# Kernel tuning notes

Measured on AMD Instinct MI355X. Metric: run time of the kernel, lower is better.

## Reference

```python
import jax, jax.numpy as jnp
import numpy as np

RMS_EPS = 1.1920928955078125e-07  # torch.finfo(float32).eps, nn.RMSNorm default when eps=None


def setup_inputs() -> dict:
    key = jax.random.key(0)
    ks = jax.random.split(key, 7)
    B, T, C, Wh, E, K = 8, 4096, 256, 1024, 8, 2
    return {
        "x": jax.random.normal(ks[0], (B, T, C), dtype=jnp.float32),
        "rms_weight": jnp.ones((C,), dtype=jnp.float32),
        "W1": jax.random.normal(ks[1], (E, C, Wh), dtype=jnp.float32),
        "b1": jax.random.normal(ks[2], (E, Wh), dtype=jnp.float32),
        "W2": jax.random.normal(ks[3], (E, Wh, C), dtype=jnp.float32),
        "b2": jax.random.normal(ks[4], (E, C), dtype=jnp.float32),
        "expert_ids": jax.random.randint(ks[5], (B, T, K), 0, E, dtype=jnp.int64),
    }


def reference(x, rms_weight, W1, b1, W2, b2, expert_ids):
    # RMSNorm over last dim (torch nn.RMSNorm, eps = float32 eps)
    xn = x * jax.lax.rsqrt(jnp.mean(x * x, axis=-1, keepdims=True) + RMS_EPS) * rms_weight
    # Per-expert 2-layer MLP. The torch code gathers per-token weight copies then bmm's;
    # mathematically identical (and far cheaper in memory) is: run every expert densely,
    # then gather the K selected expert outputs per token.
    h = jax.nn.gelu(jnp.einsum("btc,ecw->btew", xn, W1) + b1, approximate=False)  # [B,T,E,Wh]
    y = jnp.einsum("btew,ewc->btec", h, W2) + b2  # [B,T,E,C]
    # gather selected experts: [B,T,K,C]; dropout p is 0.0 (eval) -> identity
    out = jnp.take_along_axis(y, expert_ids[..., None], axis=2)
    return out
```

## Files before the change

kernel.cpp:

```cpp
#include <hip/hip_runtime.h>
#include <cstdint>

typedef unsigned short ushort_t;
typedef __bf16 bf16x8 __attribute__((ext_vector_type(8)));
typedef ushort_t u16x8 __attribute__((ext_vector_type(8)));
typedef float f32x4 __attribute__((ext_vector_type(4)));
typedef uint32_t u32x4 __attribute__((ext_vector_type(4)));

#define RMS_EPS 1.1920928955078125e-07f

__device__ __forceinline__ ushort_t f2bf(float f) {
  uint32_t u = __builtin_bit_cast(uint32_t, f);
  u += 0x7fffu + ((u >> 16) & 1u);
  return (ushort_t)(u >> 16);
}

__device__ __forceinline__ void g2l16(const ushort_t* g, ushort_t* l) {
  __builtin_amdgcn_global_load_lds(
      (const __attribute__((address_space(1))) uint32_t*)g,
      (__attribute__((address_space(3))) uint32_t*)l, 16, 0, 0);
}

__global__ void rmsnorm_cast(const float* __restrict__ x, const float* __restrict__ w,
                             ushort_t* __restrict__ xn) {
  int token = blockIdx.x * 4 + (threadIdx.x >> 6);
  int lane = threadIdx.x & 63;
  const float4* row = reinterpret_cast<const float4*>(x + (size_t)token * 256);
  float4 v = row[lane];
  float s = v.x * v.x + v.y * v.y + v.z * v.z + v.w * v.w;
#pragma unroll
  for (int off = 1; off < 64; off <<= 1) s += __shfl_xor(s, off);
  float inv = rsqrtf(s * (1.0f / 256.0f) + RMS_EPS);
  const float4* wr = reinterpret_cast<const float4*>(w);
  float4 wv = wr[lane];
  ushort4 o;
  o.x = f2bf(v.x * inv * wv.x);
  o.y = f2bf(v.y * inv * wv.y);
  o.z = f2bf(v.z * inv * wv.z);
  o.w = f2bf(v.w * inv * wv.w);
  *reinterpret_cast<ushort4*>(xn + (size_t)token * 256 + lane * 4) = o;
}

__global__ void pack_w(const float* __restrict__ W1, const float* __restrict__ W2,
                       ushort_t* __restrict__ w1f, ushort_t* __restrict__ w2f) {
  int U = blockIdx.x * 256 + threadIdx.x;
  int isW2 = (U >= 262144);
  U &= 262143;
  int lane = U & 63, l16 = lane & 15, quad = lane >> 4;
  int e = U >> 15;
  int ch = (U >> 10) & 31;
  u16x8 o;
  if (!isW2) {
    int nt = (U >> 6) & 1, kk = (U >> 7) & 7;
    const float* s = W1 + ((size_t)e << 18) +
                     (size_t)(kk * 32 + quad * 8) * 1024 + ch * 32 + nt * 16 + l16;
#pragma unroll
    for (int j = 0; j < 8; ++j) o[j] = f2bf(s[(size_t)j * 1024]);
    *reinterpret_cast<u16x8*>(w1f + (size_t)U * 8) = o;
  } else {
    int ct = (U >> 6) & 15;
    const float* s = W2 + ((size_t)e << 18) +
                     (size_t)(ch * 32 + quad * 8) * 256 + ct * 16 + l16;
#pragma unroll
    for (int j = 0; j < 8; ++j) o[j] = f2bf(s[(size_t)j * 256]);
    *reinterpret_cast<u16x8*>(w2f + (size_t)U * 8) = o;
  }
}

__global__ void route_pairs(const int* __restrict__ eids, int* __restrict__ cnt,
                            int* __restrict__ lists) {
  __shared__ int lcnt[8], lbase[8];
  int tid = threadIdx.x;
  if (tid < 8) lcnt[tid] = 0;
  __syncthreads();
  int p = blockIdx.x * 256 + tid;
  int e = eids[p];
  int lpos = atomicAdd(&lcnt[e], 1);
  __syncthreads();
  if (tid < 8) lbase[tid] = atomicAdd(&cnt[tid], lcnt[tid]);
  __syncthreads();
  lists[e * 65536 + lbase[e] + lpos] = p;
}

__global__ __launch_bounds__(256, 2) void moe_mlp(
    const ushort_t* __restrict__ xn,
    const ushort_t* __restrict__ w1f,
    const ushort_t* __restrict__ w2f,
    const float* __restrict__ b1,
    const float* __restrict__ b2,
    const int* __restrict__ cnt,
    const int* __restrict__ lists,
    float* __restrict__ out)
{
  __shared__ __align__(16) ushort_t w1b[2][8192];
  __shared__ __align__(16) ushort_t w2b[2][8192];
  __shared__ __align__(16) ushort_t hlds[4][32][40];
  __shared__ int prs[128];

  int flat = blockIdx.x;
  int e = -1, tile = 0, accum = 0, n_e = 0;
#pragma unroll
  for (int i = 0; i < 8; ++i) {
    int c = cnt[i];
    int t = (c + 127) >> 7;
    if (e < 0 && flat < accum + t) { e = i; tile = flat - accum; n_e = c; }
    accum += t;
  }
  if (e < 0) return;
  int start = tile * 128;

  int tid = threadIdx.x;
  if (tid < 128) {
    int idx = start + tid;
    prs[tid] = (idx < n_e) ? lists[e * 65536 + idx] : lists[e * 65536];
  }

  const ushort_t* w1e = w1f + ((size_t)e << 18);
  const ushort_t* w2e = w2f + ((size_t)e << 18);
  int wave = tid >> 6, lane = tid & 63, l16 = lane & 15, quad = lane >> 4;

  {
#pragma unroll
    for (int j = 0; j < 4; ++j) {
      int p = j * 4 + wave;
      g2l16(w1e + p * 512 + lane * 8, &w1b[0][p * 512]);
      g2l16(w2e + p * 512 + lane * 8, &w2b[0][p * 512]);
    }
  }
  __syncthreads();

  bf16x8 afr[2][8];
#pragma unroll
  for (int mt = 0; mt < 2; ++mt) {
    int tok = prs[wave * 32 + mt * 16 + l16] >> 1;
    const u32x4* arow = reinterpret_cast<const u32x4*>(xn + (size_t)tok * 256);
#pragma unroll
    for (int kk = 0; kk < 8; ++kk)
      afr[mt][kk] = __builtin_bit_cast(bf16x8, arow[kk * 4 + quad]);
  }

  f32x4 acc[2][16];
#pragma unroll
  for (int mt = 0; mt < 2; ++mt)
#pragma unroll
    for (int ct = 0; ct < 16; ++ct) acc[mt][ct] = (f32x4){0.f, 0.f, 0.f, 0.f};

  const float* b1e = b1 + e * 1024;

  for (int ch = 0; ch < 32; ++ch) {
    int cur = ch & 1;
    __syncthreads();
    if (ch + 1 < 32) {
      const ushort_t* n1 = w1e + (ch + 1) * 8192;
      const ushort_t* n2 = w2e + (ch + 1) * 8192;
#pragma unroll
      for (int j = 0; j < 4; ++j) {
        int p = j * 4 + wave;
        g2l16(n1 + p * 512 + lane * 8, &w1b[cur ^ 1][p * 512]);
        g2l16(n2 + p * 512 + lane * 8, &w2b[cur ^ 1][p * 512]);
      }
    }
    const ushort_t* l1 = w1b[cur];
    const ushort_t* l2 = w2b[cur];

    f32x4 h1[2][2];
    h1[0][0] = (f32x4){0.f, 0.f, 0.f, 0.f};
    h1[0][1] = (f32x4){0.f, 0.f, 0.f, 0.f};
    h1[1][0] = (f32x4){0.f, 0.f, 0.f, 0.f};
    h1[1][1] = (f32x4){0.f, 0.f, 0.f, 0.f};
#pragma unroll
    for (int kk = 0; kk < 8; ++kk) {
#pragma unroll
      for (int nt = 0; nt < 2; ++nt) {
        bf16x8 b = *reinterpret_cast<const bf16x8*>(l1 + ((kk * 2 + nt) * 64 + lane) * 8);
        h1[nt][0] = __builtin_amdgcn_mfma_f32_16x16x32_bf16(afr[0][kk], b, h1[nt][0], 0, 0, 0);
        h1[nt][1] = __builtin_amdgcn_mfma_f32_16x16x32_bf16(afr[1][kk], b, h1[nt][1], 0, 0, 0);
      }
    }

    int w0 = ch * 32;
#pragma unroll
    for (int nt = 0; nt < 2; ++nt) {
      float bias = b1e[w0 + nt * 16 + l16];
#pragma unroll
      for (int mt = 0; mt < 2; ++mt) {
#pragma unroll
        for (int r = 0; r < 4; ++r) {
          float v = h1[nt][mt][r] + bias;
          float u_ = v + 0.044715f * v * v * v;
          float q = __expf(1.5957691216f * u_);
          float g = v - v * __builtin_amdgcn_rcpf(1.0f + q);
          hlds[wave][mt * 16 + quad * 4 + r][nt * 16 + l16] = f2bf(g);
        }
      }
    }
    bf16x8 a2_0 = *reinterpret_cast<const bf16x8*>(&hlds[wave][l16][quad * 8]);
    bf16x8 a2_1 = *reinterpret_cast<const bf16x8*>(&hlds[wave][16 + l16][quad * 8]);

#pragma unroll
    for (int ct = 0; ct < 16; ++ct) {
      bf16x8 b = *reinterpret_cast<const bf16x8*>(l2 + (ct * 64 + lane) * 8);
      acc[0][ct] = __builtin_amdgcn_mfma_f32_16x16x32_bf16(a2_0, b, acc[0][ct], 0, 0, 0);
      acc[1][ct] = __builtin_amdgcn_mfma_f32_16x16x32_bf16(a2_1, b, acc[1][ct], 0, 0, 0);
    }
  }

  const float* b2e = b2 + e * 256;
  float bl[16];
#pragma unroll
  for (int ct = 0; ct < 16; ++ct) bl[ct] = b2e[ct * 16 + l16];
#pragma unroll
  for (int mt = 0; mt < 2; ++mt) {
#pragma unroll
    for (int r = 0; r < 4; ++r) {
      int m = wave * 32 + mt * 16 + quad * 4 + r;
      if (start + m < n_e) {
        float* orow = out + (size_t)prs[m] * 256;
#pragma unroll
        for (int ct = 0; ct < 16; ++ct)
          orow[ct * 16 + l16] = acc[mt][ct][r] + bl[ct];
      }
    }
  }
}

extern "C" void kernel_launch(void* const* d_in, const int* in_sizes, int n_in,
                              void* d_out, int out_size, void* d_ws, size_t ws_size,
                              hipStream_t stream) {
  const float* x  = (const float*)d_in[0];
  const float* rw = (const float*)d_in[1];
  const float* W1 = (const float*)d_in[2];
  const float* b1 = (const float*)d_in[3];
  const float* W2 = (const float*)d_in[4];
  const float* b2 = (const float*)d_in[5];
  const int* eids = (const int*)d_in[6];
  float* out = (float*)d_out;

  char* ws = (char*)d_ws;
  ushort_t* xn  = (ushort_t*)(ws);
  ushort_t* w1f = (ushort_t*)(ws + 16777216);
  ushort_t* w2f = (ushort_t*)(ws + 20971520);
  int* cnt      = (int*)(ws + 25165824);
  int* lists    = (int*)(ws + 25166080);

  hipMemsetAsync(cnt, 0, 8 * sizeof(int), stream);
  rmsnorm_cast<<<8192, 256, 0, stream>>>(x, rw, xn);
  pack_w<<<2048, 256, 0, stream>>>(W1, W2, w1f, w2f);
  route_pairs<<<256, 256, 0, stream>>>(eids, cnt, lists);
  moe_mlp<<<519, 256, 0, stream>>>(xn, w1f, w2f, b1, b2, cnt, lists, out);
}
```

Before: 268.8 us.

## Stage weight packing through LDS tile and reorder first-GEMM/GELU in MoE kernel

The weight pack kernel now reads coalesced float4 rows of W1/W2 into a shared-memory bf16 tile, then emits the MFMA fragment layout from LDS. Before, each thread made eight strided scalar loads. In the main MLP kernel, the first GEMM is split into two sequential n-tile loops and the b1 bias loads are hoisted ahead of the MFMAs. GELU is rewritten as v*sigmoid using one fewer multiply. These changes target global-memory inefficiency in packing and instruction overhead in the hot loop, at the cost of extra LDS use in packing.

```diff
diff --git a/kernel.cpp b/kernel.cpp
--- a/kernel.cpp
+++ b/kernel.cpp
@@ -41,29 +41,52 @@
   *reinterpret_cast<ushort4*>(xn + (size_t)token * 256 + lane * 4) = o;
 }
 
-__global__ void pack_w(const float* __restrict__ W1, const float* __restrict__ W2,
-                       ushort_t* __restrict__ w1f, ushort_t* __restrict__ w2f) {
-  int U = blockIdx.x * 256 + threadIdx.x;
-  int isW2 = (U >= 262144);
-  U &= 262143;
-  int lane = U & 63, l16 = lane & 15, quad = lane >> 4;
-  int e = U >> 15;
-  int ch = (U >> 10) & 31;
-  u16x8 o;
-  if (!isW2) {
-    int nt = (U >> 6) & 1, kk = (U >> 7) & 7;
-    const float* s = W1 + ((size_t)e << 18) +
-                     (size_t)(kk * 32 + quad * 8) * 1024 + ch * 32 + nt * 16 + l16;
-#pragma unroll
-    for (int j = 0; j < 8; ++j) o[j] = f2bf(s[(size_t)j * 1024]);
-    *reinterpret_cast<u16x8*>(w1f + (size_t)U * 8) = o;
-  } else {
-    int ct = (U >> 6) & 15;
-    const float* s = W2 + ((size_t)e << 18) +
-                     (size_t)(ch * 32 + quad * 8) * 256 + ct * 16 + l16;
-#pragma unroll
-    for (int j = 0; j < 8; ++j) o[j] = f2bf(s[(size_t)j * 256]);
-    *reinterpret_cast<u16x8*>(w2f + (size_t)U * 8) = o;
+__global__ __launch_bounds__(256) void pack_w(const float* __restrict__ W1,
+                                              const float* __restrict__ W2,
+                                              ushort_t* __restrict__ w1f,
+                                              ushort_t* __restrict__ w2f) {
+  __shared__ ushort_t tile[64][130];
+  int b = blockIdx.x;
+  int isW2 = b >= 256;
+  const float* src; ushort_t* dst; int e, kt, wt, rs;
+  if (!isW2) { e = b >> 5; kt = (b >> 3) & 3; wt = b & 7; src = W1; dst = w1f; rs = 1024; }
+  else { b -= 256; e = b >> 5; kt = (b >> 1) & 15; wt = b & 1; src = W2; dst = w2f; rs = 256; }
+  int k0 = kt * 64, c0 = wt * 128;
+  const float* sb = src + ((size_t)e << 18) + (size_t)k0 * rs + c0;
+  int t = threadIdx.x;
+#pragma unroll
+  for (int i = 0; i < 8; ++i) {
+    int f = i * 1024 + t * 4;
+    int r = f >> 7, c = f & 127;
+    float4 v = *reinterpret_cast<const float4*>(sb + (size_t)r * rs + c);
+    ushort2 lo, hi;
+    lo.x = f2bf(v.x); lo.y = f2bf(v.y); hi.x = f2bf(v.z); hi.y = f2bf(v.w);
+    *reinterpret_cast<ushort2*>(&tile[r][c]) = lo;
+    *reinterpret_cast<ushort2*>(&tile[r][c + 2]) = hi;
+  }
+  __syncthreads();
+  int lane = t & 63, l16 = lane & 15, quad = lane >> 4;
+#pragma unroll
+  for (int p = 0; p < 4; ++p) {
+    int u = p * 256 + t;
+    int kk2 = (u >> 9) & 1;
+    int rr = kk2 * 32 + quad * 8;
+    u16x8 o;
+    size_t U;
+    if (!isW2) {
+      int nt = (u >> 6) & 1, chL = (u >> 7) & 3;
+      int cc = chL * 32 + nt * 16 + l16;
+#pragma unroll
+      for (int j = 0; j < 8; ++j) o[j] = tile[rr + j][cc];
+      U = ((size_t)e * 32768) + (size_t)(wt * 4 + chL) * 1024 + (kt * 2 + kk2) * 128 + nt * 64 + lane;
+    } else {
+      int ntL = (u >> 6) & 7;
+      int cc = ntL * 16 + l16;
+#pragma unroll
+      for (int j = 0; j < 8; ++j) o[j] = tile[rr + j][cc];
+      U = ((size_t)e * 32768) + (size_t)(kt * 2 + kk2) * 1024 + (wt * 8 + ntL) * 64 + lane;
+    }
+    *reinterpret_cast<u16x8*>(dst + U * 8) = o;
   }
 }
 
@@ -119,13 +142,11 @@
   const ushort_t* w2e = w2f + ((size_t)e << 18);
   int wave = tid >> 6, lane = tid & 63, l16 = lane & 15, quad = lane >> 4;
 
-  {
-#pragma unroll
-    for (int j = 0; j < 4; ++j) {
-      int p = j * 4 + wave;
-      g2l16(w1e + p * 512 + lane * 8, &w1b[0][p * 512]);
-      g2l16(w2e + p * 512 + lane * 8, &w2b[0][p * 512]);
-    }
+#pragma unroll
+  for (int j = 0; j < 4; ++j) {
+    int p = j * 4 + wave;
+    g2l16(w1e + p * 512 + lane * 8, &w1b[0][p * 512]);
+    g2l16(w2e + p * 512 + lane * 8, &w2b[0][p * 512]);
   }
   __syncthreads();
 
@@ -146,6 +167,7 @@
     for (int ct = 0; ct < 16; ++ct) acc[mt][ct] = (f32x4){0.f, 0.f, 0.f, 0.f};
 
   const float* b1e = b1 + e * 1024;
+  ushort_t* hl = &hlds[wave][0][0];
 
   for (int ch = 0; ch < 32; ++ch) {
     int cur = ch & 1;
@@ -162,40 +184,63 @@
     }
     const ushort_t* l1 = w1b[cur];
     const ushort_t* l2 = w2b[cur];
-
-    f32x4 h1[2][2];
-    h1[0][0] = (f32x4){0.f, 0.f, 0.f, 0.f};
-    h1[0][1] = (f32x4){0.f, 0.f, 0.f, 0.f};
-    h1[1][0] = (f32x4){0.f, 0.f, 0.f, 0.f};
-    h1[1][1] = (f32x4){0.f, 0.f, 0.f, 0.f};
+    int w0 = ch * 32;
+    float bias0 = b1e[w0 + l16];
+    float bias1 = b1e[w0 + 16 + l16];
+
+    f32x4 h00 = (f32x4){0.f, 0.f, 0.f, 0.f};
+    f32x4 h01 = (f32x4){0.f, 0.f, 0.f, 0.f};
+    f32x4 h10 = (f32x4){0.f, 0.f, 0.f, 0.f};
+    f32x4 h11 = (f32x4){0.f, 0.f, 0.f, 0.f};
 #pragma unroll
     for (int kk = 0; kk < 8; ++kk) {
-#pragma unroll
-      for (int nt = 0; nt < 2; ++nt) {
-        bf16x8 b = *reinterpret_cast<const bf16x8*>(l1 + ((kk * 2 + nt) * 64 + lane) * 8);
-        h1[nt][0] = __builtin_amdgcn_mfma_f32_16x16x32_bf16(afr[0][kk], b, h1[nt][0], 0, 0, 0);
-        h1[nt][1] = __builtin_amdgcn_mfma_f32_16x16x32_bf16(afr[1][kk], b, h1[nt][1], 0, 0, 0);
-      }
-    }
-
-    int w0 = ch * 32;
-#pragma unroll
-    for (int nt = 0; nt < 2; ++nt) {
-      float bias = b1e[w0 + nt * 16 + l16];
-#pragma unroll
-      for (int mt = 0; mt < 2; ++mt) {
-#pragma unroll
-        for (int r = 0; r < 4; ++r) {
-          float v = h1[nt][mt][r] + bias;
-          float u_ = v + 0.044715f * v * v * v;
-          float q = __expf(1.5957691216f * u_);
-          float g = v - v * __builtin_amdgcn_rcpf(1.0f + q);
-          hlds[wave][mt * 16 + quad * 4 + r][nt * 16 + l16] = f2bf(g);
-        }
-      }
-    }
-    bf16x8 a2_0 = *reinterpret_cast<const bf16x8*>(&hlds[wave][l16][quad * 8]);
-    bf16x8 a2_1 = *reinterpret_cast<const bf16x8*>(&hlds[wave][16 + l16][quad * 8]);
+      bf16x8 bA = *reinterpret_cast<const bf16x8*>(l1 + ((kk * 2 + 0) * 64 + lane) * 8);
+      h00 = __builtin_amdgcn_mfma_f32_16x16x32_bf16(afr[0][kk], bA, h00, 0, 0, 0);
+      h01 = __builtin_amdgcn_mfma_f32_16x16x32_bf16(afr[1][kk], bA, h01, 0, 0, 0);
+    }
+#pragma unroll
+    for (int kk = 0; kk < 8; ++kk) {
+      bf16x8 bB = *reinterpret_cast<const bf16x8*>(l1 + ((kk * 2 + 1) * 64 + lane) * 8);
+      h10 = __builtin_amdgcn_mfma_f32_16x16x32_bf16(afr[0][kk], bB, h10, 0, 0, 0);
+      h11 = __builtin_amdgcn_mfma_f32_16x16x32_bf16(afr[1][kk], bB, h11, 0, 0, 0);
+    }
+#pragma unroll
+    for (int r = 0; r < 4; ++r) {
+      {
+        float v = h00[r] + bias0;
+        float v2 = v * v;
+        float u_ = (0.044715f * v2) * v + v;
+        float tq = __expf(-1.5957691216057308f * u_);
+        float g = v * __builtin_amdgcn_rcpf(1.0f + tq);
+        hl[(quad * 4 + r) * 40 + l16] = f2bf(g);
+      }
+      {
+        float v = h01[r] + bias0;
+        float v2 = v * v;
+        float u_ = (0.044715f * v2) * v + v;
+        float tq = __expf(-1.5957691216057308f * u_);
+        float g = v * __builtin_amdgcn_rcpf(1.0f + tq);
+        hl[(16 + quad * 4 + r) * 40 + l16] = f2bf(g);
+      }
+      {
+        float v = h10[r] + bias1;
+        float v2 = v * v;
+        float u_ = (0.044715f * v2) * v + v;
+        float tq = __expf(-1.5957691216057308f * u_);
+        float g = v * __builtin_amdgcn_rcpf(1.0f + tq);
+        hl[(quad * 4 + r) * 40 + 16 + l16] = f2bf(g);
+      }
+      {
+        float v = h11[r] + bias1;
+        float v2 = v * v;
+        float u_ = (0.044715f * v2) * v + v;
+        float tq = __expf(-1.5957691216057308f * u_);
+        float g = v * __builtin_amdgcn_rcpf(1.0f + tq);
+        hl[(16 + quad * 4 + r) * 40 + 16 + l16] = f2bf(g);
+      }
+    }
+    bf16x8 a2_0 = *reinterpret_cast<const bf16x8*>(hl + l16 * 40 + quad * 8);
+    bf16x8 a2_1 = *reinterpret_cast<const bf16x8*>(hl + (16 + l16) * 40 + quad * 8);
 
 #pragma unroll
     for (int ct = 0; ct < 16; ++ct) {
@@ -245,7 +290,7 @@
 
   hipMemsetAsync(cnt, 0, 8 * sizeof(int), stream);
   rmsnorm_cast<<<8192, 256, 0, stream>>>(x, rw, xn);
-  pack_w<<<2048, 256, 0, stream>>>(W1, W2, w1f, w2f);
+  pack_w<<<512, 256, 0, stream>>>(W1, W2, w1f, w2f);
   route_pairs<<<256, 256, 0, stream>>>(eids, cnt, lists);
   moe_mlp<<<519, 256, 0, stream>>>(xn, w1f, w2f, b1, b2, cnt, lists, out);
 }
```

New measurement: 253.3 us. 1.06x faster.
